# Performance work log

Measured on AMD Instinct MI355X. Metric: run time of the kernel, lower is better.

Reference implementation:

```python
import jax, jax.numpy as jnp
import numpy as np

# BlendParams defaults (pytorch3d) and camera clip planes from the module
SIGMA = 1e-4
GAMMA = 1e-4
BACKGROUND = (1.0, 1.0, 1.0)
ZNEAR = 1.0
ZFAR = 100.0
EPS = 1e-10

N, H, W, K = 4, 512, 512, 8
F, V = 100000, 50000


def setup_inputs() -> dict:
    key = jax.random.key(0)
    k1, k2, k3, k4, k5, k6 = jax.random.split(key, 6)
    bary = jax.random.uniform(k1, (N, H, W, K, 3), dtype=jnp.float32)
    bary = bary / jnp.sum(bary, axis=-1, keepdims=True)  # valid barycentric coords
    # depth buffer values inside [znear, zfar]
    zbuf = ZNEAR + (ZFAR - ZNEAR) * jax.random.uniform(k2, (N, H, W, K), dtype=jnp.float32)
    # signed squared distances to face edges, small magnitude (rasterizer blur region)
    dists = 1e-4 * jax.random.normal(k3, (N, H, W, K), dtype=jnp.float32)
    vn = jax.random.normal(k4, (V, 3), dtype=jnp.float32)
    verts_normals = vn / jnp.linalg.norm(vn, axis=-1, keepdims=True)
    # -1 marks background pixels (no face rasterized into that slot)
    pix_to_face = jax.random.randint(k5, (N, H, W, K), -1, F, dtype=jnp.int32)
    faces = jax.random.randint(k6, (F, 3), 0, V, dtype=jnp.int32)
    return {
        "bary_coords": bary,
        "zbuf": zbuf,
        "dists": dists,
        "verts_normals": verts_normals,
        "pix_to_face": pix_to_face,
        "faces": faces,
    }


def _shade_and_blend(bary_coords, zbuf, dists, verts_normals, pix_to_face, faces):
    mask = pix_to_face >= 0                       # [N,H,W,K]
    p2f = jnp.where(mask, pix_to_face, 0)
    # world_normal_shading: interpolate_face_attributes(pix_to_face, bary, verts_normals[faces])
    face_vert_normals = verts_normals[faces]      # [F,3,3] (3 verts, 3 components)
    pix_attrs = face_vert_normals[p2f]            # [N,H,W,K,3,3]
    colors = jnp.einsum("nhwkv,nhwkvc->nhwkc", bary_coords, pix_attrs)
    colors = jnp.where(mask[..., None], colors, 0.0)  # zero out empty fragments

    # softmax_rgb_blend (pytorch3d)
    maskf = mask.astype(colors.dtype)
    prob_map = jax.nn.sigmoid(-dists / SIGMA) * maskf          # [N,H,W,K]
    alpha = 1.0 - jnp.prod(1.0 - prob_map, axis=-1)            # [N,H,W]
    z_inv = (ZFAR - zbuf) / (ZFAR - ZNEAR) * maskf             # [N,H,W,K]
    z_inv_max = jnp.maximum(jnp.max(z_inv, axis=-1, keepdims=True), EPS)
    weights_num = prob_map * jnp.exp((z_inv - z_inv_max) / GAMMA)
    delta = jnp.exp((EPS - z_inv_max) / GAMMA)                 # [N,H,W,1]
    denom = jnp.sum(weights_num, axis=-1, keepdims=True) + delta
    weighted_colors = jnp.einsum("nhwk,nhwkc->nhwc", weights_num, colors) / denom
    background = jnp.asarray(BACKGROUND, dtype=colors.dtype)
    weighted_background = (delta / denom) * background         # [N,H,W,3]
    rgb = weighted_colors + weighted_background
    return jnp.concatenate([rgb, alpha[..., None]], axis=-1)   # [N,H,W,4]


def reference(bary_coords, zbuf, dists, verts_normals, pix_to_face, faces):
    return _shade_and_blend(bary_coords, zbuf, dists, verts_normals, pix_to_face, faces)
```

## Files before the change

### kernel.cpp

```cpp
#include <hip/hip_runtime.h>

#define K 8

typedef float    f32x4 __attribute__((ext_vector_type(4)));
typedef int      i32x4 __attribute__((ext_vector_type(4)));
typedef unsigned u32x4 __attribute__((ext_vector_type(4)));

static __device__ __forceinline__ unsigned quant10(float v) {
    v = fminf(fmaxf(v, -1.0f), 1.0f);
    return (unsigned)__float2uint_rn((v + 1.0f) * 511.5f);
}

__global__ __launch_bounds__(256) void pack_face_normals_q10(
    const int*   __restrict__ faces,
    const float* __restrict__ vn,
    u32x4*       __restrict__ tbl,
    int F)
{
    int f = blockIdx.x * blockDim.x + threadIdx.x;
    if (f >= F) return;
    int v0 = faces[3 * f + 0];
    int v1 = faces[3 * f + 1];
    int v2 = faces[3 * f + 2];
    u32x4 r;
    r.x = quant10(vn[3 * v0 + 0]) | (quant10(vn[3 * v0 + 1]) << 10) | (quant10(vn[3 * v0 + 2]) << 20);
    r.y = quant10(vn[3 * v1 + 0]) | (quant10(vn[3 * v1 + 1]) << 10) | (quant10(vn[3 * v1 + 2]) << 20);
    r.z = quant10(vn[3 * v2 + 0]) | (quant10(vn[3 * v2 + 1]) << 10) | (quant10(vn[3 * v2 + 2]) << 20);
    r.w = 0u;
    tbl[f] = r;
}

static __device__ __forceinline__ float dq(unsigned w, int shift) {
    const float S = 2.0f / 1023.0f;
    return (float)((w >> shift) & 1023u) * S - 1.0f;
}

__global__ __launch_bounds__(256) void shade_blend_q10(
    const float* __restrict__ bary,
    const float* __restrict__ zbuf,
    const float* __restrict__ dists,
    const int*   __restrict__ p2f,
    const u32x4* __restrict__ tbl,
    float*       __restrict__ out,
    int P)
{
    const float SIGMA_INV = 1e4f;
    const float GAMMA_INV = 1e4f;
    const float EPSV      = 1e-10f;
    const float ZFAR      = 100.0f;
    const float ZSCALE    = 1.0f / 99.0f;

    int pix = blockIdx.x * blockDim.x + threadIdx.x;
    if (pix >= P) return;

    const f32x4* zb4 = reinterpret_cast<const f32x4*>(zbuf  + (size_t)pix * K);
    const f32x4* ds4 = reinterpret_cast<const f32x4*>(dists + (size_t)pix * K);
    const i32x4* pf4 = reinterpret_cast<const i32x4*>(p2f   + (size_t)pix * K);
    const f32x4* bc4 = reinterpret_cast<const f32x4*>(bary  + (size_t)pix * K * 3);

    f32x4 za  = __builtin_nontemporal_load(zb4 + 0);
    f32x4 zb_ = __builtin_nontemporal_load(zb4 + 1);
    f32x4 da  = __builtin_nontemporal_load(ds4 + 0);
    f32x4 db_ = __builtin_nontemporal_load(ds4 + 1);
    i32x4 fa  = __builtin_nontemporal_load(pf4 + 0);
    i32x4 fb_ = __builtin_nontemporal_load(pf4 + 1);

    float zk[K] = { za.x, za.y, za.z, za.w, zb_.x, zb_.y, zb_.z, zb_.w };
    float dk[K] = { da.x, da.y, da.z, da.w, db_.x, db_.y, db_.z, db_.w };
    int   fk[K] = { fa.x, fa.y, fa.z, fa.w, fb_.x, fb_.y, fb_.z, fb_.w };

    float barr[K * 3];
#pragma unroll
    for (int i = 0; i < 6; ++i) {
        f32x4 t = __builtin_nontemporal_load(bc4 + i);
        barr[4 * i + 0] = t.x;
        barr[4 * i + 1] = t.y;
        barr[4 * i + 2] = t.z;
        barr[4 * i + 3] = t.w;
    }

    u32x4 rec[K];
#pragma unroll
    for (int k = 0; k < K; ++k) {
        int fi = fk[k] >= 0 ? fk[k] : 0;
        rec[k] = tbl[fi];
    }

    float prob[K], zinv[K], c0[K], c1[K], c2[K];
    float zmax = EPSV;

#pragma unroll
    for (int k = 0; k < K; ++k) {
        float mf = fk[k] >= 0 ? 1.0f : 0.0f;

        float p = 1.0f / (1.0f + __expf(dk[k] * SIGMA_INV));
        prob[k] = p * mf;
        zinv[k] = (ZFAR - zk[k]) * ZSCALE * mf;
        zmax = fmaxf(zmax, zinv[k]);

        unsigned w0 = rec[k].x, w1 = rec[k].y, w2 = rec[k].z;
        float b0 = barr[3 * k + 0] * mf;
        float b1 = barr[3 * k + 1] * mf;
        float b2 = barr[3 * k + 2] * mf;
        c0[k] = b0 * dq(w0, 0)  + b1 * dq(w1, 0)  + b2 * dq(w2, 0);
        c1[k] = b0 * dq(w0, 10) + b1 * dq(w1, 10) + b2 * dq(w2, 10);
        c2[k] = b0 * dq(w0, 20) + b1 * dq(w1, 20) + b2 * dq(w2, 20);
    }

    float one_minus_prod = 1.0f;
    float wsum = 0.0f, a0 = 0.0f, a1 = 0.0f, a2 = 0.0f;
#pragma unroll
    for (int k = 0; k < K; ++k) {
        one_minus_prod *= (1.0f - prob[k]);
        float w = prob[k] * __expf((zinv[k] - zmax) * GAMMA_INV);
        wsum += w;
        a0 += w * c0[k];
        a1 += w * c1[k];
        a2 += w * c2[k];
    }
    float delta = __expf((EPSV - zmax) * GAMMA_INV);
    float inv_denom = 1.0f / (wsum + delta);
    float bgw = delta * inv_denom;

    f32x4 o;
    o.x = a0 * inv_denom + bgw;
    o.y = a1 * inv_denom + bgw;
    o.z = a2 * inv_denom + bgw;
    o.w = 1.0f - one_minus_prod;
    __builtin_nontemporal_store(o, reinterpret_cast<f32x4*>(out + (size_t)pix * 4));
}

__global__ __launch_bounds__(256) void shade_blend_direct(
    const float* __restrict__ bary, const float* __restrict__ zbuf,
    const float* __restrict__ dists, const float* __restrict__ vn,
    const int* __restrict__ p2f, const int* __restrict__ faces,
    float* __restrict__ out, int P)
{
    const float SIGMA_INV = 1e4f, GAMMA_INV = 1e4f, EPSV = 1e-10f;
    const float ZFAR = 100.0f, ZSCALE = 1.0f / 99.0f;
    int pix = blockIdx.x * blockDim.x + threadIdx.x;
    if (pix >= P) return;
    const float4* zb4 = reinterpret_cast<const float4*>(zbuf  + (size_t)pix * K);
    const float4* ds4 = reinterpret_cast<const float4*>(dists + (size_t)pix * K);
    const int4*   pf4 = reinterpret_cast<const int4*>(p2f     + (size_t)pix * K);
    const float4* bc4 = reinterpret_cast<const float4*>(bary  + (size_t)pix * K * 3);
    float4 za = zb4[0], zb_ = zb4[1];
    float4 da = ds4[0], db_ = ds4[1];
    int4   fa = pf4[0], fb_ = pf4[1];
    float zk[K] = { za.x, za.y, za.z, za.w, zb_.x, zb_.y, zb_.z, zb_.w };
    float dk[K] = { da.x, da.y, da.z, da.w, db_.x, db_.y, db_.z, db_.w };
    int   fk[K] = { fa.x, fa.y, fa.z, fa.w, fb_.x, fb_.y, fb_.z, fb_.w };
    float barr[K * 3];
#pragma unroll
    for (int i = 0; i < 6; ++i) {
        float4 t = bc4[i];
        barr[4 * i + 0] = t.x; barr[4 * i + 1] = t.y;
        barr[4 * i + 2] = t.z; barr[4 * i + 3] = t.w;
    }
    float prob[K], zinv[K], c0[K], c1[K], c2[K];
    float zmax = EPSV;
#pragma unroll
    for (int k = 0; k < K; ++k) {
        int fraw = fk[k];
        float mf = fraw >= 0 ? 1.0f : 0.0f;
        int fi = fraw >= 0 ? fraw : 0;
        int v0 = faces[3 * fi + 0], v1 = faces[3 * fi + 1], v2 = faces[3 * fi + 2];
        float p = 1.0f / (1.0f + __expf(dk[k] * SIGMA_INV));
        prob[k] = p * mf;
        zinv[k] = (ZFAR - zk[k]) * ZSCALE * mf;
        zmax = fmaxf(zmax, zinv[k]);
        float b0 = barr[3 * k + 0] * mf, b1 = barr[3 * k + 1] * mf, b2 = barr[3 * k + 2] * mf;
        c0[k] = b0 * vn[3 * v0 + 0] + b1 * vn[3 * v1 + 0] + b2 * vn[3 * v2 + 0];
        c1[k] = b0 * vn[3 * v0 + 1] + b1 * vn[3 * v1 + 1] + b2 * vn[3 * v2 + 1];
        c2[k] = b0 * vn[3 * v0 + 2] + b1 * vn[3 * v1 + 2] + b2 * vn[3 * v2 + 2];
    }
    float one_minus_prod = 1.0f, wsum = 0.0f, a0 = 0.0f, a1 = 0.0f, a2 = 0.0f;
#pragma unroll
    for (int k = 0; k < K; ++k) {
        one_minus_prod *= (1.0f - prob[k]);
        float w = prob[k] * __expf((zinv[k] - zmax) * GAMMA_INV);
        wsum += w; a0 += w * c0[k]; a1 += w * c1[k]; a2 += w * c2[k];
    }
    float delta = __expf((EPSV - zmax) * GAMMA_INV);
    float inv_denom = 1.0f / (wsum + delta);
    float bgw = delta * inv_denom;
    float4 o;
    o.x = a0 * inv_denom + bgw; o.y = a1 * inv_denom + bgw;
    o.z = a2 * inv_denom + bgw; o.w = 1.0f - one_minus_prod;
    *reinterpret_cast<float4*>(out + (size_t)pix * 4) = o;
}

extern "C" void kernel_launch(void* const* d_in, const int* in_sizes, int n_in,
                              void* d_out, int out_size, void* d_ws, size_t ws_size,
                              hipStream_t stream) {
    const float* bary  = (const float*)d_in[0];
    const float* zbuf  = (const float*)d_in[1];
    const float* dists = (const float*)d_in[2];
    const float* vn    = (const float*)d_in[3];
    const int*   p2f   = (const int*)d_in[4];
    const int*   faces = (const int*)d_in[5];
    float* out = (float*)d_out;

    int P = out_size / 4;
    int F = in_sizes[5] / 3;
    int block = 256;
    int grid = (P + block - 1) / block;

    size_t tbl_bytes = (size_t)F * 16;
    if (ws_size >= tbl_bytes) {
        u32x4* tbl = (u32x4*)d_ws;
        int gf = (F + block - 1) / block;
        pack_face_normals_q10<<<gf, block, 0, stream>>>(faces, vn, tbl, F);
        shade_blend_q10<<<grid, block, 0, stream>>>(bary, zbuf, dists, p2f, tbl, out, P);
    } else {
        shade_blend_direct<<<grid, block, 0, stream>>>(bary, zbuf, dists, vn, p2f, faces, out, P);
    }
}
```

Before: 279.1 us.

## Map one thread per fragment with wave shuffles for per-pixel blend reductions

Switches the shading kernel from one thread per pixel to one thread per fragment (8 lanes per pixel). The max, sum and product reductions over K are done with xor shuffles, and lanes 0-3 each store one output channel. This aims to raise occupancy and the number of concurrent table gathers, at the cost of extra shuffles, scalar instead of 128-bit loads and stores, and redundant tail math in every lane.

```diff
diff --git a/kernel.cpp b/kernel.cpp
--- a/kernel.cpp
+++ b/kernel.cpp
@@ -3,12 +3,15 @@
 #define K 8
 
 typedef float    f32x4 __attribute__((ext_vector_type(4)));
-typedef int      i32x4 __attribute__((ext_vector_type(4)));
 typedef unsigned u32x4 __attribute__((ext_vector_type(4)));
 
 static __device__ __forceinline__ unsigned quant10(float v) {
     v = fminf(fmaxf(v, -1.0f), 1.0f);
     return (unsigned)__float2uint_rn((v + 1.0f) * 511.5f);
+}
+static __device__ __forceinline__ float dq(unsigned w, int shift) {
+    const float S = 2.0f / 1023.0f;
+    return (float)((w >> shift) & 1023u) * S - 1.0f;
 }
 
 __global__ __launch_bounds__(256) void pack_face_normals_q10(
@@ -30,19 +33,14 @@
     tbl[f] = r;
 }
 
-static __device__ __forceinline__ float dq(unsigned w, int shift) {
-    const float S = 2.0f / 1023.0f;
-    return (float)((w >> shift) & 1023u) * S - 1.0f;
-}
-
-__global__ __launch_bounds__(256) void shade_blend_q10(
+__global__ __launch_bounds__(256) void shade_blend_frag(
     const float* __restrict__ bary,
     const float* __restrict__ zbuf,
     const float* __restrict__ dists,
     const int*   __restrict__ p2f,
     const u32x4* __restrict__ tbl,
     float*       __restrict__ out,
-    int P)
+    int total)
 {
     const float SIGMA_INV = 1e4f;
     const float GAMMA_INV = 1e4f;
@@ -50,84 +48,60 @@
     const float ZFAR      = 100.0f;
     const float ZSCALE    = 1.0f / 99.0f;
 
-    int pix = blockIdx.x * blockDim.x + threadIdx.x;
-    if (pix >= P) return;
+    int tid = blockIdx.x * blockDim.x + threadIdx.x;
+    if (tid >= total) return;
+    int pix = tid >> 3;
+    int k   = tid & 7;
 
-    const f32x4* zb4 = reinterpret_cast<const f32x4*>(zbuf  + (size_t)pix * K);
-    const f32x4* ds4 = reinterpret_cast<const f32x4*>(dists + (size_t)pix * K);
-    const i32x4* pf4 = reinterpret_cast<const i32x4*>(p2f   + (size_t)pix * K);
-    const f32x4* bc4 = reinterpret_cast<const f32x4*>(bary  + (size_t)pix * K * 3);
+    int   f = __builtin_nontemporal_load(p2f   + tid);
+    float z = __builtin_nontemporal_load(zbuf  + tid);
+    float d = __builtin_nontemporal_load(dists + tid);
+    const float* bb = bary + (size_t)tid * 3;
+    float b0 = __builtin_nontemporal_load(bb + 0);
+    float b1 = __builtin_nontemporal_load(bb + 1);
+    float b2 = __builtin_nontemporal_load(bb + 2);
 
-    f32x4 za  = __builtin_nontemporal_load(zb4 + 0);
-    f32x4 zb_ = __builtin_nontemporal_load(zb4 + 1);
-    f32x4 da  = __builtin_nontemporal_load(ds4 + 0);
-    f32x4 db_ = __builtin_nontemporal_load(ds4 + 1);
-    i32x4 fa  = __builtin_nontemporal_load(pf4 + 0);
-    i32x4 fb_ = __builtin_nontemporal_load(pf4 + 1);
+    int fi = f >= 0 ? f : 0;
+    u32x4 rec = tbl[fi];
+    float mf = f >= 0 ? 1.0f : 0.0f;
 
-    float zk[K] = { za.x, za.y, za.z, za.w, zb_.x, zb_.y, zb_.z, zb_.w };
-    float dk[K] = { da.x, da.y, da.z, da.w, db_.x, db_.y, db_.z, db_.w };
-    int   fk[K] = { fa.x, fa.y, fa.z, fa.w, fb_.x, fb_.y, fb_.z, fb_.w };
+    float p    = 1.0f / (1.0f + __expf(d * SIGMA_INV));
+    float prob = p * mf;
+    float zinv = (ZFAR - z) * ZSCALE * mf;
+    b0 *= mf; b1 *= mf; b2 *= mf;
+    float c0 = b0 * dq(rec.x, 0)  + b1 * dq(rec.y, 0)  + b2 * dq(rec.z, 0);
+    float c1 = b0 * dq(rec.x, 10) + b1 * dq(rec.y, 10) + b2 * dq(rec.z, 10);
+    float c2 = b0 * dq(rec.x, 20) + b1 * dq(rec.y, 20) + b2 * dq(rec.z, 20);
 
-    float barr[K * 3];
+    float zmax = fmaxf(zinv, EPSV);
+    zmax = fmaxf(zmax, __shfl_xor(zmax, 1));
+    zmax = fmaxf(zmax, __shfl_xor(zmax, 2));
+    zmax = fmaxf(zmax, __shfl_xor(zmax, 4));
+
+    float w  = prob * __expf((zinv - zmax) * GAMMA_INV);
+    float a0 = w * c0, a1 = w * c1, a2 = w * c2;
+    float pm = 1.0f - prob;
+
 #pragma unroll
-    for (int i = 0; i < 6; ++i) {
-        f32x4 t = __builtin_nontemporal_load(bc4 + i);
-        barr[4 * i + 0] = t.x;
-        barr[4 * i + 1] = t.y;
-        barr[4 * i + 2] = t.z;
-        barr[4 * i + 3] = t.w;
+    for (int m = 1; m <= 4; m <<= 1) {
+        w  += __shfl_xor(w,  m);
+        a0 += __shfl_xor(a0, m);
+        a1 += __shfl_xor(a1, m);
+        a2 += __shfl_xor(a2, m);
+        pm *= __shfl_xor(pm, m);
     }
 
-    u32x4 rec[K];
-#pragma unroll
-    for (int k = 0; k < K; ++k) {
-        int fi = fk[k] >= 0 ? fk[k] : 0;
-        rec[k] = tbl[fi];
+    float delta = __expf((EPSV - zmax) * GAMMA_INV);
+    float invd  = 1.0f / (w + delta);
+    float bgw   = delta * invd;
+
+    if (k < 4) {
+        float val = (k == 0) ? a0 * invd + bgw
+                  : (k == 1) ? a1 * invd + bgw
+                  : (k == 2) ? a2 * invd + bgw
+                  :            1.0f - pm;
+        __builtin_nontemporal_store(val, out + (size_t)pix * 4 + k);
     }
-
-    float prob[K], zinv[K], c0[K], c1[K], c2[K];
-    float zmax = EPSV;
-
-#pragma unroll
-    for (int k = 0; k < K; ++k) {
-        float mf = fk[k] >= 0 ? 1.0f : 0.0f;
-
-        float p = 1.0f / (1.0f + __expf(dk[k] * SIGMA_INV));
-        prob[k] = p * mf;
-        zinv[k] = (ZFAR - zk[k]) * ZSCALE * mf;
-        zmax = fmaxf(zmax, zinv[k]);
-
-        unsigned w0 = rec[k].x, w1 = rec[k].y, w2 = rec[k].z;
-        float b0 = barr[3 * k + 0] * mf;
-        float b1 = barr[3 * k + 1] * mf;
-        float b2 = barr[3 * k + 2] * mf;
-        c0[k] = b0 * dq(w0, 0)  + b1 * dq(w1, 0)  + b2 * dq(w2, 0);
-        c1[k] = b0 * dq(w0, 10) + b1 * dq(w1, 10) + b2 * dq(w2, 10);
-        c2[k] = b0 * dq(w0, 20) + b1 * dq(w1, 20) + b2 * dq(w2, 20);
-    }
-
-    float one_minus_prod = 1.0f;
-    float wsum = 0.0f, a0 = 0.0f, a1 = 0.0f, a2 = 0.0f;
-#pragma unroll
-    for (int k = 0; k < K; ++k) {
-        one_minus_prod *= (1.0f - prob[k]);
-        float w = prob[k] * __expf((zinv[k] - zmax) * GAMMA_INV);
-        wsum += w;
-        a0 += w * c0[k];
-        a1 += w * c1[k];
-        a2 += w * c2[k];
-    }
-    float delta = __expf((EPSV - zmax) * GAMMA_INV);
-    float inv_denom = 1.0f / (wsum + delta);
-    float bgw = delta * inv_denom;
-
-    f32x4 o;
-    o.x = a0 * inv_denom + bgw;
-    o.y = a1 * inv_denom + bgw;
-    o.z = a2 * inv_denom + bgw;
-    o.w = 1.0f - one_minus_prod;
-    __builtin_nontemporal_store(o, reinterpret_cast<f32x4*>(out + (size_t)pix * 4));
 }
 
 __global__ __launch_bounds__(256) void shade_blend_direct(
@@ -160,26 +134,26 @@
     float prob[K], zinv[K], c0[K], c1[K], c2[K];
     float zmax = EPSV;
 #pragma unroll
-    for (int k = 0; k < K; ++k) {
-        int fraw = fk[k];
+    for (int kk = 0; kk < K; ++kk) {
+        int fraw = fk[kk];
         float mf = fraw >= 0 ? 1.0f : 0.0f;
         int fi = fraw >= 0 ? fraw : 0;
         int v0 = faces[3 * fi + 0], v1 = faces[3 * fi + 1], v2 = faces[3 * fi + 2];
-        float p = 1.0f / (1.0f + __expf(dk[k] * SIGMA_INV));
-        prob[k] = p * mf;
-        zinv[k] = (ZFAR - zk[k]) * ZSCALE * mf;
-        zmax = fmaxf(zmax, zinv[k]);
-        float b0 = barr[3 * k + 0] * mf, b1 = barr[3 * k + 1] * mf, b2 = barr[3 * k + 2] * mf;
-        c0[k] = b0 * vn[3 * v0 + 0] + b1 * vn[3 * v1 + 0] + b2 * vn[3 * v2 + 0];
-        c1[k] = b0 * vn[3 * v0 + 1] + b1 * vn[3 * v1 + 1] + b2 * vn[3 * v2 + 1];
-        c2[k] = b0 * vn[3 * v0 + 2] + b1 * vn[3 * v1 + 2] + b2 * vn[3 * v2 + 2];
+        float p = 1.0f / (1.0f + __expf(dk[kk] * SIGMA_INV));
+        prob[kk] = p * mf;
+        zinv[kk] = (ZFAR - zk[kk]) * ZSCALE * mf;
+        zmax = fmaxf(zmax, zinv[kk]);
+        float b0 = barr[3 * kk + 0] * mf, b1 = barr[3 * kk + 1] * mf, b2 = barr[3 * kk + 2] * mf;
+        c0[kk] = b0 * vn[3 * v0 + 0] + b1 * vn[3 * v1 + 0] + b2 * vn[3 * v2 + 0];
+        c1[kk] = b0 * vn[3 * v0 + 1] + b1 * vn[3 * v1 + 1] + b2 * vn[3 * v2 + 1];
+        c2[kk] = b0 * vn[3 * v0 + 2] + b1 * vn[3 * v1 + 2] + b2 * vn[3 * v2 + 2];
     }
     float one_minus_prod = 1.0f, wsum = 0.0f, a0 = 0.0f, a1 = 0.0f, a2 = 0.0f;
 #pragma unroll
-    for (int k = 0; k < K; ++k) {
-        one_minus_prod *= (1.0f - prob[k]);
-        float w = prob[k] * __expf((zinv[k] - zmax) * GAMMA_INV);
-        wsum += w; a0 += w * c0[k]; a1 += w * c1[k]; a2 += w * c2[k];
+    for (int kk = 0; kk < K; ++kk) {
+        one_minus_prod *= (1.0f - prob[kk]);
+        float w = prob[kk] * __expf((zinv[kk] - zmax) * GAMMA_INV);
+        wsum += w; a0 += w * c0[kk]; a1 += w * c1[kk]; a2 += w * c2[kk];
     }
     float delta = __expf((EPSV - zmax) * GAMMA_INV);
     float inv_denom = 1.0f / (wsum + delta);
@@ -204,15 +178,17 @@
     int P = out_size / 4;
     int F = in_sizes[5] / 3;
     int block = 256;
-    int grid = (P + block - 1) / block;
 
     size_t tbl_bytes = (size_t)F * 16;
     if (ws_size >= tbl_bytes) {
         u32x4* tbl = (u32x4*)d_ws;
         int gf = (F + block - 1) / block;
         pack_face_normals_q10<<<gf, block, 0, stream>>>(faces, vn, tbl, F);
-        shade_blend_q10<<<grid, block, 0, stream>>>(bary, zbuf, dists, p2f, tbl, out, P);
+        int total = P * K;
+        int grid = (total + block - 1) / block;
+        shade_blend_frag<<<grid, block, 0, stream>>>(bary, zbuf, dists, p2f, tbl, out, total);
     } else {
+        int grid = (P + block - 1) / block;
         shade_blend_direct<<<grid, block, 0, stream>>>(bary, zbuf, dists, vn, p2f, faces, out, P);
     }
 }
```

After: 250.6 us. -10.2%, faster.
